# Kernel optimization log

Hardware: AMD Instinct MI355X
Metric: run time of the kernel (lower is better)

Reference implementation:

```python
import jax, jax.numpy as jnp
import numpy as np

D = 128           # embed_dim
NUM_LAYERS = 2
N_CLASSES = 4
OUT_CELL = 64
SPEAKERS = 2
INPUT_DIMS = [768, 74, 35]
B, T = 32, 60


def setup_inputs() -> dict:
    key = jax.random.key(0)
    ks = jax.random.split(key, 24)
    inp = {}
    inp['x0'] = jax.random.normal(ks[0], (B, T, INPUT_DIMS[0]), jnp.float32)
    inp['x1'] = jax.random.normal(ks[1], (B, T, INPUT_DIMS[1]), jnp.float32)
    inp['x2'] = jax.random.normal(ks[2], (B, T, INPUT_DIMS[2]), jnp.float32)
    inp['smask'] = jax.random.normal(ks[3], (B, T, SPEAKERS), jnp.float32)  # argmax -> speaker ids
    # modality projections
    for i, d in enumerate(INPUT_DIMS):
        inp[f'Wp{i}'] = jax.random.normal(ks[4 + i], (d, D), jnp.float32) / np.float32(np.sqrt(d))
        inp[f'bp{i}'] = jnp.zeros((D,), jnp.float32)
    # shared PositionEmbedding (ModuleList([m]*3) shares params)
    inp['freq_emb'] = jax.random.normal(ks[7], (SPEAKERS, D), jnp.float32) * 0.1
    inp['phase_emb'] = jax.random.normal(ks[8], (SPEAKERS, D), jnp.float32)
    # shared QRNNCell (ModuleList([cell]*num_layers) shares params)
    inp['U_x'] = jnp.linalg.qr(jax.random.normal(ks[9], (D, D), jnp.float32))[0]
    inp['U_h'] = jnp.linalg.qr(jax.random.normal(ks[10], (D, D), jnp.float32))[0]
    inp['Lambda'] = jnp.float32(0.5)
    # QMeasurement kernel (real/imag parts of D measurement vectors)
    inp['kernel_r'] = jnp.eye(D, dtype=jnp.float32) + 0.05 * jax.random.normal(ks[11], (D, D), jnp.float32)
    inp['kernel_i'] = 0.05 * jax.random.normal(ks[12], (D, D), jnp.float32)
    # SimpleNet fc_out
    inp['W1'] = jax.random.normal(ks[13], (D, OUT_CELL), jnp.float32) / np.float32(np.sqrt(D))
    inp['b1'] = jnp.zeros((OUT_CELL,), jnp.float32)
    inp['W2'] = jax.random.normal(ks[14], (OUT_CELL, N_CLASSES), jnp.float32) / np.float32(np.sqrt(OUT_CELL))
    inp['b2'] = jnp.zeros((N_CLASSES,), jnp.float32)
    return inp


def _qmn_forward(x0, x1, x2, smask, Wp0, bp0, Wp1, bp1, Wp2, bp2,
                 freq_emb, phase_emb, U_x, U_h, Lambda,
                 kernel_r, kernel_i, W1, b1, W2, b2):
    xs = [x0, x1, x2]
    Ws = [(Wp0, bp0), (Wp1, bp1), (Wp2, bp2)]
    reps = [jax.nn.relu(x @ W + b) for x, (W, b) in zip(xs, Ws)]           # [B,T,D] each
    # mixture weights: softmax over per-modality L2 norms
    norms = jnp.concatenate([jnp.linalg.norm(r, axis=-1, keepdims=True) for r in reps], axis=-1)
    weights = jax.nn.softmax(norms, axis=-1)                               # [B,T,M]
    # shared phase embedding: phase = t * freq[speaker] + phase[speaker]
    ids = jnp.argmax(smask, axis=-1)                                       # [B,T] int
    pos = jnp.arange(T, dtype=jnp.float32)[None, :, None]                  # [1,T,1]
    phase = pos * freq_emb[ids] + phase_emb[ids]                           # [B,T,D]
    cosp, sinp = jnp.cos(phase), jnp.sin(phase)
    # mixed density matrices rho = sum_m w_m |v_m><v_m|
    rho_r = jnp.zeros((B, T, D, D), jnp.float32)
    rho_i = jnp.zeros((B, T, D, D), jnp.float32)
    for m, r in enumerate(reps):
        a = r / jnp.maximum(jnp.linalg.norm(r, axis=-1, keepdims=True), 1e-12)
        pr = a * cosp                                                       # real amplitude
        pi = a * sinp                                                       # imag amplitude
        w = weights[..., m][..., None, None]
        rho_r = rho_r + w * (jnp.einsum('btm,btn->btmn', pr, pr) + jnp.einsum('btm,btn->btmn', pi, pi))
        rho_i = rho_i + w * (jnp.einsum('btm,btn->btmn', pi, pr) - jnp.einsum('btm,btn->btmn', pr, pi))
    # time-major for scan
    sr = jnp.transpose(rho_r, (1, 0, 2, 3))                                # [T,B,D,D]
    si = jnp.transpose(rho_i, (1, 0, 2, 3))

    def cell(h, x):
        hr, hi = h
        xr, xi = x
        Xr = jnp.einsum('mp,bpq,nq->bmn', U_x, xr, U_x)
        Xi = jnp.einsum('mp,bpq,nq->bmn', U_x, xi, U_x)
        Hr = jnp.einsum('mp,bpq,nq->bmn', U_h, hr, U_h)
        Hi = jnp.einsum('mp,bpq,nq->bmn', U_h, hi, U_h)
        nr = Lambda * Hr + (1.0 - Lambda) * Xr
        ni = Lambda * Hi + (1.0 - Lambda) * Xi
        return (nr, ni), (nr, ni)

    h0 = (jnp.broadcast_to(jnp.eye(D, dtype=jnp.float32) / D, (B, D, D)),
          jnp.zeros((B, D, D), jnp.float32))
    for _ in range(NUM_LAYERS):  # same shared cell params each layer
        _, (sr, si) = jax.lax.scan(cell, h0, (sr, si))
    # QMeasurement: p_k = Re(v_k^dag rho v_k), unit-norm complex measurement vectors
    nrm = jnp.sqrt(jnp.sum(kernel_r**2 + kernel_i**2, axis=1, keepdims=True))
    vr = kernel_r / jnp.maximum(nrm, 1e-12)                                # [K,D], K=D
    vi = kernel_i / jnp.maximum(nrm, 1e-12)
    probs = (jnp.einsum('tbmn,km,kn->tbk', sr, vr, vr)
             + jnp.einsum('tbmn,km,kn->tbk', sr, vi, vi)
             - jnp.einsum('tbmn,km,kn->tbk', si, vr, vi)
             + jnp.einsum('tbmn,km,kn->tbk', si, vi, vr))                  # [T,B,D]
    # SimpleNet (dropout = identity at inference)
    hid = jax.nn.relu(probs @ W1 + b1)
    out = jnp.tanh(hid @ W2 + b2)                                          # [T,B,C]
    out = jnp.transpose(out, (1, 0, 2))                                    # [B,T,C]
    return jax.nn.log_softmax(out, axis=2)


def reference(x0, x1, x2, smask, Wp0, bp0, Wp1, bp1, Wp2, bp2,
              freq_emb, phase_emb, U_x, U_h, Lambda,
              kernel_r, kernel_i, W1, b1, W2, b2):
    return _qmn_forward(x0, x1, x2, smask, Wp0, bp0, Wp1, bp1, Wp2, bp2,
                        freq_emb, phase_emb, U_x, U_h, Lambda,
                        kernel_r, kernel_i, W1, b1, W2, b2)
```

## Files before the change

### kernel.cpp

```cpp
#include <hip/hip_runtime.h>


#define DB 32
#define DT 60
#define DD 128
#define BT (DB*DT)
#define SP 136

typedef unsigned short ushort_t;
typedef __attribute__((ext_vector_type(8))) __bf16 bf16x8;
typedef __attribute__((ext_vector_type(8))) unsigned short ushort8_t;
typedef __attribute__((ext_vector_type(4))) float  float4v;

__device__ __forceinline__ float bf2f(ushort_t u){
  union { unsigned int i; float f; } x; x.i = ((unsigned int)u) << 16; return x.f;
}
__device__ __forceinline__ ushort_t f2bf(float f){
  union { float f; unsigned int i; } x; x.f = f;
  unsigned int lsb = (x.i >> 16) & 1u;
  return (ushort_t)((x.i + 0x7FFFu + lsb) >> 16);
}
__device__ __forceinline__ unsigned int f2bfpk(float a, float b){
#if defined(__gfx950__) && __has_builtin(__builtin_amdgcn_cvt_pk_bf16_f32)
  auto v = __builtin_amdgcn_cvt_pk_bf16_f32(a, b);
  unsigned int r; __builtin_memcpy(&r, &v, 4); return r;
#else
  return (unsigned int)f2bf(a) | ((unsigned int)f2bf(b) << 16);
#endif
}
__device__ __forceinline__ void split2(float v, ushort_t& h, ushort_t& l){
  h = f2bf(v); l = f2bf(v - bf2f(h));
}

template<int RT, int CT, bool ALO, bool BLO>
__device__ __forceinline__ void gemm_t(const ushort_t* Ah, const ushort_t* Al,
                                       const ushort_t* Bh, const ushort_t* Bl,
                                       float4v* acc, int row0, int col0, int gma, int q)
{
  for (int ks = 0; ks < 4; ks++){
    int ko = ks*32 + q*8;
    bf16x8 aF[RT], aL[RT], bF[CT], bL[CT];
    #pragma unroll
    for (int R = 0; R < RT; R++){
      int row = row0 + 16*R + gma;
      aF[R] = *(const bf16x8*)&Ah[row*SP + ko];
      if (ALO) aL[R] = *(const bf16x8*)&Al[row*SP + ko];
    }
    #pragma unroll
    for (int C = 0; C < CT; C++){
      int row = col0 + 16*C + gma;
      bF[C] = *(const bf16x8*)&Bh[row*SP + ko];
      if (BLO) bL[C] = *(const bf16x8*)&Bl[row*SP + ko];
    }
    #pragma unroll
    for (int R = 0; R < RT; R++)
      #pragma unroll
      for (int C = 0; C < CT; C++){
        float4v c = acc[R*CT+C];
        c = __builtin_amdgcn_mfma_f32_16x16x32_bf16(aF[R], bF[C], c, 0, 0, 0);
        if (BLO) c = __builtin_amdgcn_mfma_f32_16x16x32_bf16(aF[R], bL[C], c, 0, 0, 0);
        if (ALO) c = __builtin_amdgcn_mfma_f32_16x16x32_bf16(aL[R], bF[C], c, 0, 0, 0);
        acc[R*CT+C] = c;
      }
  }
}

template<int RT, int CT>
__device__ __forceinline__ void emit_t(const float4v* acc, ushort_t* dst, int stride,
                                       int row0, int col0, int gma, int q){
  #pragma unroll
  for (int R = 0; R < RT; R++)
    #pragma unroll
    for (int C = 0; C < CT; C++){
      int c = col0 + 16*C + gma, r0 = row0 + 16*R + 4*q;
      uint2 o;
      o.x = f2bfpk(acc[R*CT+C][0], acc[R*CT+C][1]);
      o.y = f2bfpk(acc[R*CT+C][2], acc[R*CT+C][3]);
      *(uint2*)&dst[(size_t)c*stride + r0] = o;
    }
}
template<int RT, int CT>
__device__ __forceinline__ void emit_split_t(const float4v* acc, ushort_t* dh, ushort_t* dl, int stride,
                                             int row0, int col0, int gma, int q){
  #pragma unroll
  for (int R = 0; R < RT; R++)
    #pragma unroll
    for (int C = 0; C < CT; C++){
      int c = col0 + 16*C + gma, r0 = row0 + 16*R + 4*q;
      ushort4 hh, ll;
      split2(acc[R*CT+C][0], hh.x, ll.x); split2(acc[R*CT+C][1], hh.y, ll.y);
      split2(acc[R*CT+C][2], hh.z, ll.z); split2(acc[R*CT+C][3], hh.w, ll.w);
      *(ushort4*)&dh[(size_t)c*stride + r0] = hh;
      *(ushort4*)&dl[(size_t)c*stride + r0] = ll;
    }
}
template<int NT>
__device__ __forceinline__ void lds_load_mat(ushort_t* dst, const ushort_t* src, int tid){
  for (int i = tid*8; i < 16384; i += NT*8){
    int r = i >> 7, k = i & 127;
    *(ushort8_t*)&dst[r*SP + k] = *(const ushort8_t*)&src[i];
  }
}
template<int NT>
__device__ __forceinline__ void lds_load_rows16(ushort_t* dst, const ushort_t* src, int tid){
  for (int i = tid*8; i < 2048; i += NT*8){
    int r = i >> 7, k = i & 127;
    *(ushort8_t*)&dst[r*SP + k] = *(const ushort8_t*)&src[i];
  }
}
template<int NT>
__device__ __forceinline__ void lds_load_mat2(ushort_t* d0, const ushort_t* s0,
                                              ushort_t* d1, const ushort_t* s1, int tid){
  constexpr int CH = 16384/(NT*8);
  ushort8_t r0[CH], r1[CH];
  #pragma unroll
  for (int c = 0; c < CH; c++) r0[c] = *(const ushort8_t*)&s0[tid*8 + c*NT*8];
  #pragma unroll
  for (int c = 0; c < CH; c++) r1[c] = *(const ushort8_t*)&s1[tid*8 + c*NT*8];
  #pragma unroll
  for (int c = 0; c < CH; c++){
    int i = tid*8 + c*NT*8; int r = i >> 7, k = i & 127;
    *(ushort8_t*)&d0[r*SP + k] = r0[c];
  }
  #pragma unroll
  for (int c = 0; c < CH; c++){
    int i = tid*8 + c*NT*8; int r = i >> 7, k = i & 127;
    *(ushort8_t*)&d1[r*SP + k] = r1[c];
  }
}
template<int NT>
__device__ __forceinline__ void lds_store_mat(ushort_t* dst, const ushort_t* src, int tid){
  for (int i = tid*8; i < 16384; i += NT*8){
    int r = i >> 7, k = i & 127;
    *(ushort8_t*)&dst[i] = *(const ushort8_t*)&src[r*SP + k];
  }
}

__device__ __forceinline__ void pow2_body(int blk2, int s,
    ushort_t* PpH, ushort_t* PpL, ushort_t* PTh, ushort_t* PTl,
    int tid, ushort_t* Ah, ushort_t* Al, ushort_t* Bh, ushort_t* Bl)
{
  int which = blk2 >> 3, sl = blk2 & 7;
  size_t src = (size_t)(s-1)*16384, dst = (size_t)s*16384;
  int gcol0 = sl*16;
  const ushort_t *A_h, *A_l, *B_h, *B_l; ushort_t *D_h, *D_l;
  if (which == 0){ A_h = PTh+src; A_l = PTl+src; B_h = PpH+src; B_l = PpL+src;
                   D_h = PpH+dst; D_l = PpL+dst; }
  else           { A_h = PpH+src; A_l = PpL+src; B_h = PTh+src; B_l = PTl+src;
                   D_h = PTh+dst; D_l = PTl+dst; }
  if (tid < 256){
    lds_load_mat<256>(Ah, A_h, tid);
    lds_load_mat<256>(Al, A_l, tid);
    lds_load_rows16<256>(Bh, B_h + (size_t)gcol0*128, tid);
    lds_load_rows16<256>(Bl, B_l + (size_t)gcol0*128, tid);
  }
  __syncthreads();
  if (tid < 256){
    int w = tid >> 6, lane = tid & 63, gma = lane & 15, q = lane >> 4;
    int row0 = 32*w;
    float4v acc[2];
    acc[0] = (float4v){0.f,0.f,0.f,0.f};
    acc[1] = (float4v){0.f,0.f,0.f,0.f};
    gemm_t<2,1,true,true>(Ah, Al, Bh, Bl, acc, row0, 0, gma, q);
    emit_split_t<2,1>(acc, D_h, D_l, 128, row0, gcol0, gma, q);
  }
}

__global__ void k_small(const float* Ux, const float* Uh, const float* kr, const float* ki,
                        const float* Wp0, const float* Wp1, const float* Wp2,
                        const float* x0, const float* x1, const float* x2,
                        ushort_t* UxTh, ushort_t* UxTl, ushort_t* UxH, ushort_t* UxL,
                        float* Vr, float* Vi,
                        ushort_t* PpH, ushort_t* PpL, ushort_t* PTh, ushort_t* PTl,
                        ushort_t* WT0h, ushort_t* WT0l, ushort_t* WT1h, ushort_t* WT1l,
                        ushort_t* WT2h, ushort_t* WT2l,
                        ushort_t* X0h, ushort_t* X0l, ushort_t* X1h, ushort_t* X1l,
                        ushort_t* X2h, ushort_t* X2l){
  int blk = blockIdx.x, d = threadIdx.x;
  if (blk < 128){
    int i = blk;
    float v = Ux[i*DD + d];
    ushort_t h, l; split2(v, h, l);
    UxTh[d*DD + i] = h; UxTl[d*DD + i] = l;
  } else if (blk < 256){
    __shared__ float red[DD];
    int k = blk - 128;
    float r = kr[k*DD+d], im = ki[k*DD+d];
    red[d] = r*r + im*im;
    __syncthreads();
    for (int s = 64; s > 0; s >>= 1){ if (d < s) red[d] += red[d+s]; __syncthreads(); }
    float nrm = fmaxf(sqrtf(red[0]), 1e-12f);
    Vr[k*DD+d] = r/nrm; Vi[k*DD+d] = im/nrm;
  } else if (blk < 384){
    int i = blk - 256;
    float v = Uh[i*DD + d];
    ushort_t h, l; split2(v, h, l);
    PpH[i*DD + d] = h;  PpL[i*DD + d] = l;
    PTh[d*DD + i] = h;  PTl[d*DD + i] = l;
  } else if (blk < 512){
    int dd2 = blk - 384;
    ushort_t h, l;
    for (int k = d; k < 768; k += 128){
      split2(Wp0[(size_t)k*DD + dd2], h, l);
      WT0h[(size_t)dd2*768 + k] = h; WT0l[(size_t)dd2*768 + k] = l;
    }
    { float v = (d < 74) ? Wp1[(size_t)d*DD + dd2] : 0.f;
      split2(v, h, l); WT1h[dd2*128 + d] = h; WT1l[dd2*128 + d] = l; }
    { float v = (d < 35) ? Wp2[(size_t)d*DD + dd2] : 0.f;
      split2(v, h, l); WT2h[dd2*128 + d] = h; WT2l[dd2*128 + d] = l; }
    { split2(Ux[(size_t)dd2*DD + d], h, l);
      UxH[dd2*DD + d] = h; UxL[dd2*DD + d] = l; }
  } else {
    int bt = blk - 512;
    ushort_t h, l;
    const float* r0 = x0 + (size_t)bt*768;
    #pragma unroll
    for (int j = 0; j < 6; j++){
      split2(r0[j*128 + d], h, l);
      X0h[(size_t)bt*768 + j*128 + d] = h;
      X0l[(size_t)bt*768 + j*128 + d] = l;
    }
    float v1 = (d < 74) ? x1[(size_t)bt*74 + d] : 0.f;
    split2(v1, h, l);
    X1h[(size_t)bt*128 + d] = h; X1l[(size_t)bt*128 + d] = l;
    float v2 = (d < 35) ? x2[(size_t)bt*35 + d] : 0.f;
    split2(v2, h, l);
    X2h[(size_t)bt*128 + d] = h; X2l[(size_t)bt*128 + d] = l;
  }
}

__global__ __launch_bounds__(512,1) void k_proj(
    const ushort_t* X0h, const ushort_t* X0l, const ushort_t* X1h, const ushort_t* X1l,
    const ushort_t* X2h, const ushort_t* X2l,
    const ushort_t* WT0h, const ushort_t* WT0l, const ushort_t* WT1h, const ushort_t* WT1l,
    const ushort_t* WT2h, const ushort_t* WT2l,
    const float* bp1, const float* bp2,
    float* Rpart, float* Reps,
    ushort_t* PpH, ushort_t* PpL, ushort_t* PTh, ushort_t* PTl)
{
  __shared__ ushort_t Ah[128*SP], Al[128*SP], Bh[128*SP], Bl[128*SP];
  int blk = blockIdx.x;
  int tid = threadIdx.x;
  if (blk >= 120){
    pow2_body(blk - 120, 1, PpH, PpL, PTh, PTl, tid, Ah, Al, Bh, Bl);
    return;
  }
  int m, tile, ch;
  if (blk < 90){ m = 0; tile = blk/6; ch = blk%6; }
  else if (blk < 105){ m = 1; tile = blk-90; ch = 0; }
  else { m = 2; tile = blk-105; ch = 0; }
  int bt0 = tile*128;
  int w = tid >> 6, lane = tid & 63, gma = lane & 15, q = lane >> 4;
  int row0 = 32*(w >> 1), col0 = 64*(w & 1);
  const ushort_t* Wh_ = (m==0)? WT0h : (m==1)? WT1h : WT2h;
  const ushort_t* Wl_ = (m==0)? WT0l : (m==1)? WT1l : WT2l;
  const ushort_t* Xh_ = (m==0)? X0h : (m==1)? X1h : X2h;
  const ushort_t* Xl_ = (m==0)? X0l : (m==1)? X1l : X2l;
  int KX = (m==0)? 768 : 128;
  for (int i = tid*8; i < 16384; i += 4096){
    int r = i >> 7, k = i & 127;
    *(ushort8_t*)&Ah[r*SP + k] = *(const ushort8_t*)&Wh_[(size_t)r*KX + ch*128 + k];
    *(ushort8_t*)&Al[r*SP + k] = *(const ushort8_t*)&Wl_[(size_t)r*KX + ch*128 + k];
    *(ushort8_t*)&Bh[r*SP + k] = *(const ushort8_t*)&Xh_[(size_t)(bt0+r)*KX + ch*128 + k];
    *(ushort8_t*)&Bl[r*SP + k] = *(const ushort8_t*)&Xl_[(size_t)(bt0+r)*KX + ch*128 + k];
  }
  __syncthreads();
  float4v acc[8];
  #pragma unroll
  for (int i = 0; i < 8; i++) acc[i] = (float4v){0.f,0.f,0.f,0.f};
  gemm_t<2,4,true,true>(Ah, Al, Bh, Bl, acc, row0, col0, gma, q);
  if (m == 0){
    #pragma unroll
    for (int R = 0; R < 2; R++)
      #pragma unroll
      for (int C = 0; C < 4; C++){
        int c = col0 + 16*C + gma, r0 = row0 + 16*R + 4*q;
        float4 o;
        o.x = acc[R*4+C][0]; o.y = acc[R*4+C][1];
        o.z = acc[R*4+C][2]; o.w = acc[R*4+C][3];
        *(float4*)&Rpart[((size_t)ch*BT + bt0 + c)*128 + r0] = o;
      }
  } else {
    const float* bp = (m==1)? bp1 : bp2;
    #pragma unroll
    for (int R = 0; R < 2; R++){
      int r0 = row0 + 16*R + 4*q;
      float4 bv = *(const float4*)&bp[r0];
      #pragma unroll
      for (int C = 0; C < 4; C++){
        int c = col0 + 16*C + gma;
        float4v a = acc[R*4+C];
        float4 o;
        o.x = fmaxf(a[0]+bv.x, 0.f); o.y = fmaxf(a[1]+bv.y, 0.f);
        o.z = fmaxf(a[2]+bv.z, 0.f); o.w = fmaxf(a[3]+bv.w, 0.f);
        *(float4*)&Reps[(size_t)(bt0 + c)*384 + m*128 + r0] = o;
      }
    }
  }
}

__global__ __launch_bounds__(128) void k_mix(const float* Rpart, const float* Reps,
    const float* bp0, const float* smask,
    const float* freq, const float* phem, ushort_t* PsH, ushort_t* PsL, float* Wgt)
{
  __shared__ float part[2][3];
  int bt = blockIdx.x; int t = bt % DT;
  int d = threadIdx.x;
  float r0v = bp0[d];
  #pragma unroll
  for (int ch = 0; ch < 6; ch++)
    r0v += Rpart[((size_t)ch*BT + bt)*128 + d];
  r0v = fmaxf(r0v, 0.f);
  float r1v = Reps[(size_t)bt*384 + 128 + d];
  float r2v = Reps[(size_t)bt*384 + 256 + d];
  float s0 = r0v*r0v, s1 = r1v*r1v, s2 = r2v*r2v;
  #pragma unroll
  for (int off = 1; off < 64; off <<= 1){
    s0 += __shfl_xor(s0, off, 64);
    s1 += __shfl_xor(s1, off, 64);
    s2 += __shfl_xor(s2, off, 64);
  }
  int wv = d >> 6;
  if ((d & 63) == 0){ part[wv][0] = s0; part[wv][1] = s1; part[wv][2] = s2; }
  __syncthreads();
  float n0 = sqrtf(part[0][0] + part[1][0]);
  float n1 = sqrtf(part[0][1] + part[1][1]);
  float n2 = sqrtf(part[0][2] + part[1][2]);
  float mx = fmaxf(n0, fmaxf(n1, n2));
  float e0 = expf(n0-mx), e1 = expf(n1-mx), e2 = expf(n2-mx);
  float einv = 1.f/(e0+e1+e2);
  if (d < 3) Wgt[bt*3+d] = (d==0?e0:(d==1?e1:e2))*einv;
  float sm0 = smask[bt*2], sm1 = smask[bt*2+1];
  int id = (sm1 > sm0) ? 1 : 0;
  float ph = (float)t * freq[id*DD+d] + phem[id*DD+d];
  float cp = cosf(ph), sp = sinf(ph);
  float a0 = r0v / fmaxf(n0, 1e-12f);
  float a1 = r1v / fmaxf(n1, 1e-12f);
  float a2 = r2v / fmaxf(n2, 1e-12f);
  ushort_t h, l;
  split2(a0*cp, h, l); PsH[((size_t)0*BT + bt)*DD + d] = h; PsL[((size_t)0*BT + bt)*DD + d] = l;
  split2(a1*cp, h, l); PsH[((size_t)1*BT + bt)*DD + d] = h; PsL[((size_t)1*BT + bt)*DD + d] = l;
  split2(a2*cp, h, l); PsH[((size_t)2*BT + bt)*DD + d] = h; PsL[((size_t)2*BT + bt)*DD + d] = l;
  split2(a0*sp, h, l); PsH[((size_t)3*BT + bt)*DD + d] = h; PsL[((size_t)3*BT + bt)*DD + d] = l;
  split2(a1*sp, h, l); PsH[((size_t)4*BT + bt)*DD + d] = h; PsL[((size_t)4*BT + bt)*DD + d] = l;
  split2(a2*sp, h, l); PsH[((size_t)5*BT + bt)*DD + d] = h; PsL[((size_t)5*BT + bt)*DD + d] = l;
}

__global__ __launch_bounds__(512,1) void k_qtrans(const ushort_t* UxH, const ushort_t* UxL,
                                                  const ushort_t* PsH, const ushort_t* PsL,
                                                  ushort_t* Qb,
                                                  ushort_t* PpH, ushort_t* PpL,
                                                  ushort_t* PTh, ushort_t* PTl){
  __shared__ ushort_t Ah[128*SP], Al[128*SP], Bh[128*SP], Bl[128*SP];
  int blk = blockIdx.x;
  int tid = threadIdx.x;
  if (blk >= 90){
    pow2_body(blk - 90, 2, PpH, PpL, PTh, PTl, tid, Ah, Al, Bh, Bl);
    return;
  }
  int w = tid >> 6, lane = tid & 63, gma = lane & 15, q = lane >> 4;
  int row0 = 32*(w >> 1), col0 = 64*(w & 1);
  size_t rbase = (size_t)blk*128*128;
  lds_load_mat<512>(Ah, UxH, tid);
  lds_load_mat<512>(Al, UxL, tid);
  lds_load_mat<512>(Bh, PsH + rbase, tid);
  lds_load_mat<512>(Bl, PsL + rbase, tid);
  __syncthreads();
  float4v acc[8];
  #pragma unroll
  for (int i = 0; i < 8; i++) acc[i] = (float4v){0.f,0.f,0.f,0.f};
  gemm_t<2,4,true,true>(Ah, Al, Bh, Bl, acc, row0, col0, gma, q);
  emit_t<2,4>(acc, Qb + rbase, 128, row0, col0, gma, q);
}

__global__ __launch_bounds__(256,2) void k_pow2v2(ushort_t* PpH, ushort_t* PpL,
                                                  ushort_t* PTh, ushort_t* PTl, int s){
  __shared__ ushort_t Ah[128*SP], Al[128*SP], Bh[16*SP], Bl[16*SP];
  int blk = blockIdx.x;
  int which = blk >> 3, sl = blk & 7;
  size_t src = (size_t)(s-1)*16384, dst = (size_t)s*16384;
  int tid = threadIdx.x;
  int w = tid >> 6, lane = tid & 63, gma = lane & 15, q = lane >> 4;
  int row0 = 32*w;
  int gcol0 = sl*16;
  const ushort_t *A_h, *A_l, *B_h, *B_l; ushort_t *D_h, *D_l;
  if (which == 0){ A_h = PTh+src; A_l = PTl+src; B_h = PpH+src; B_l = PpL+src;
                   D_h = PpH+dst; D_l = PpL+dst; }
  else           { A_h = PpH+src; A_l = PpL+src; B_h = PTh+src; B_l = PTl+src;
                   D_h = PTh+dst; D_l = PTl+dst; }
  lds_load_mat<256>(Ah, A_h, tid);
  lds_load_mat<256>(Al, A_l, tid);
  lds_load_rows16<256>(Bh, B_h + (size_t)gcol0*128, tid);
  lds_load_rows16<256>(Bl, B_l + (size_t)gcol0*128, tid);
  __syncthreads();
  float4v acc[2];
  acc[0] = (float4v){0.f,0.f,0.f,0.f};
  acc[1] = (float4v){0.f,0.f,0.f,0.f};
  gemm_t<2,1,true,true>(Ah, Al, Bh, Bl, acc, row0, 0, gma, q);
  emit_split_t<2,1>(acc, D_h, D_l, 128, row0, gcol0, gma, q);
}

__global__ __launch_bounds__(512,1) void k_gchain(const ushort_t* PpH, const ushort_t* PpL,
                                                  const ushort_t* PTh, const ushort_t* PTl,
                                                  ushort_t* GTh, ushort_t* GTl){
  __shared__ ushort_t Ah[128*SP], Al[128*SP], Bh[128*SP], Bl[128*SP];
  int t = blockIdx.x;
  int tid = threadIdx.x;
  int w = tid >> 6, lane = tid & 63, gma = lane & 15, q = lane >> 4;
  int row0 = 32*(w >> 1), col0 = 64*(w & 1);
  size_t gslot = (size_t)t * 16384;
  if (t == 0){
    for (int i = tid*4; i < 16384; i += 2048){
      int r = i >> 7, k = i & 127;
      ushort4 zz; zz.x = zz.y = zz.z = zz.w = 0;
      *(ushort4*)&GTl[gslot + i] = zz;
      ushort4 oh;
      oh.x = (r == (k+0)) ? (ushort_t)0x3F80 : (ushort_t)0;
      oh.y = (r == (k+1)) ? (ushort_t)0x3F80 : (ushort_t)0;
      oh.z = (r == (k+2)) ? (ushort_t)0x3F80 : (ushort_t)0;
      oh.w = (r == (k+3)) ? (ushort_t)0x3F80 : (ushort_t)0;
      *(ushort4*)&GTh[gslot + i] = oh;
    }
    return;
  }
  int b0 = __ffs(t) - 1;
  int rem = t & ~(1 << b0);
  if (rem == 0){
    size_t ps = (size_t)b0 * 16384;
    for (int i = tid*4; i < 16384; i += 2048){
      *(ushort4*)&GTh[gslot + i] = *(const ushort4*)&PTh[ps + i];
      *(ushort4*)&GTl[gslot + i] = *(const ushort4*)&PTl[ps + i];
    }
    return;
  }
  lds_load_mat<512>(Ah, PpH + (size_t)b0*16384, tid);
  lds_load_mat<512>(Al, PpL + (size_t)b0*16384, tid);
  while (rem){
    int k = __ffs(rem) - 1;
    rem &= ~(1 << k);
    lds_load_mat<512>(Bh, PTh + (size_t)k*16384, tid);
    lds_load_mat<512>(Bl, PTl + (size_t)k*16384, tid);
    __syncthreads();
    float4v acc[8];
    #pragma unroll
    for (int i = 0; i < 8; i++) acc[i] = (float4v){0.f,0.f,0.f,0.f};
    if (rem){
      gemm_t<2,4,true,true>(Bh, Bl, Ah, Al, acc, row0, col0, gma, q);
      __syncthreads();
      emit_split_t<2,4>(acc, Ah, Al, SP, row0, col0, gma, q);
      __syncthreads();
    } else {
      gemm_t<2,4,true,true>(Ah, Al, Bh, Bl, acc, row0, col0, gma, q);
      emit_split_t<2,4>(acc, GTh + gslot, GTl + gslot, 128, row0, col0, gma, q);
    }
  }
}

__global__ __launch_bounds__(512,1) void k_mwvt(
    const ushort_t* GTh, const ushort_t* GTl,
    const ushort_t* UxTh, const ushort_t* UxTl,
    const float* Vr, const float* Vi,
    const ushort_t* Qb,
    ushort_t* Mh, ushort_t* Wh, ushort_t* At)
{
  __shared__ ushort_t LBUF[4*128*SP];
  int blk = blockIdx.x;
  int tid = threadIdx.x;
  if (blk < 180){
    ushort_t* Bh = LBUF;
    ushort_t* Bl = LBUF + 128*SP;
    ushort_t* Ah = LBUF + 2*128*SP;
    ushort_t* Al = LBUF + 3*128*SP;
    int w = tid >> 6, lane = tid & 63, gma = lane & 15, q = lane >> 4;
    int row0 = 64*(w >> 1), col0 = 64*(w & 1);
    if (blk < 60){
      int t = blk;
      if (tid < 256){
        lds_load_mat<256>(Bh, GTh + (size_t)t*16384, tid);
        lds_load_mat<256>(Bl, GTl + (size_t)t*16384, tid);
        lds_load_mat<256>(Ah, UxTh, tid);
        lds_load_mat<256>(Al, UxTl, tid);
      }
      __syncthreads();
      float4v acc[16];
      if (tid < 256){
        #pragma unroll
        for (int i = 0; i < 16; i++) acc[i] = (float4v){0.f,0.f,0.f,0.f};
        gemm_t<4,4,true,true>(Ah, Al, Bh, Bl, acc, row0, col0, gma, q);
      }
      __syncthreads();
      if (tid < 256) emit_split_t<4,4>(acc, Ah, Al, SP, row0, col0, gma, q);
      __syncthreads();
      if (tid < 256){
        #pragma unroll
        for (int i = 0; i < 16; i++) acc[i] = (float4v){0.f,0.f,0.f,0.f};
        gemm_t<4,4,true,true>(Bh, Bl, Ah, Al, acc, row0, col0, gma, q);
        #pragma unroll
        for (int R = 0; R < 4; R++)
          #pragma unroll
          for (int C = 0; C < 4; C++){
            int c = col0 + 16*C + gma, r0 = row0 + 16*R + 4*q;
            uint2 o;
            o.x = f2bfpk(acc[R*4+C][0], acc[R*4+C][1]);
            o.y = f2bfpk(acc[R*4+C][2], acc[R*4+C][3]);
            *(uint2*)&Mh[(size_t)t*16384 + c*128 + r0] = o;
          }
      }
    } else {
      int bx = blk - 60;
      int t = bx >> 1, which = bx & 1;
      if (tid < 256){
        lds_load_mat<256>(Ah, GTh + (size_t)t*16384, tid);
        lds_load_mat<256>(Al, GTl + (size_t)t*16384, tid);
        const float* V = which ? Vi : Vr;
        for (int i = tid; i < 16384; i += 256){
          int r = i >> 7, k = i & 127;
          ushort_t h, l; split2(V[i], h, l);
          Bh[r*SP + k] = h; Bl[r*SP + k] = l;
        }
      }
      __syncthreads();
      if (tid < 256){
        float4v acc[16];
        #pragma unroll
        for (int i = 0; i < 16; i++) acc[i] = (float4v){0.f,0.f,0.f,0.f};
        gemm_t<4,4,true,true>(Ah, Al, Bh, Bl, acc, row0, col0, gma, q);
        #pragma unroll
        for (int R = 0; R < 4; R++)
          #pragma unroll
          for (int C = 0; C < 4; C++){
            int c = col0 + 16*C + gma, r0 = row0 + 16*R + 4*q;
            uint2 o;
            o.x = f2bfpk(acc[R*4+C][0], acc[R*4+C][1]);
            o.y = f2bfpk(acc[R*4+C][2], acc[R*4+C][3]);
            *(uint2*)&Wh[(size_t)bx*16384 + c*128 + r0] = o;
          }
      }
    }
  } else {
    ushort_t* Ah = LBUF;
    ushort_t* Bs = LBUF + 128*SP;
    int t = blk - 180;
    int w = tid >> 6, lane = tid & 63, gma = lane & 15, q = lane >> 4;
    int row0 = (w & 3)*32, col0 = (w >> 2)*96;
    lds_load_mat<512>(Ah, GTh + (size_t)t*16384, tid);
    for (int i = tid*8; i < 192*128; i += 4096){
      int m = i >> 7, k = i & 127;
      int j = m >> 5, b = m & 31;
      *(ushort8_t*)&Bs[m*SP + k] =
        *(const ushort8_t*)&Qb[((size_t)(j*BT) + b*DT + t)*DD + k];
    }
    __syncthreads();
    float4v acc[12];
    #pragma unroll
    for (int i = 0; i < 12; i++) acc[i] = (float4v){0.f,0.f,0.f,0.f};
    gemm_t<2,6,false,false>(Ah, Ah, Bs, Bs, acc, row0, col0, gma, q);
    emit_t<2,6>(acc, At + (size_t)t*24576, 128, row0, col0, gma, q);
  }
}

__global__ __launch_bounds__(256) void k_zbuild(ushort_t* S, const ushort_t* At,
                                                const float* Wgt, const float* lamp){
  __shared__ ushort_t As[2][6*DD];
  __shared__ float wl[2][3];
  int blk = blockIdx.x;
  int b = blk >> 5, sl2 = blk & 31;
  int tid = threadIdx.x;
  int r = sl2*4 + (tid >> 6);
  int c = (tid*2) & 127;
  float lam = lamp[0];
  float z0 = 0.f, z1 = 0.f;
  size_t off = (size_t)sl2*512 + tid*2;
  ushort4 pre;
  float wpre = 0.f;
  int jj0 = 0, n0 = 0;
  if (tid < 192){
    int i = tid*4;
    jj0 = i >> 7; n0 = i & 127;
    pre = *(const ushort4*)&At[(size_t)(jj0*32 + b)*128 + n0];
  }
  if (tid < 3) wpre = Wgt[(b*DT)*3 + tid];
  for (int t = 0; t < DT; t++){
    int cur = t & 1;
    if (tid < 192) *(ushort4*)&As[cur][tid*4] = pre;
    if (tid < 3) wl[cur][tid] = wpre;
    __syncthreads();
    if (t+1 < DT){
      if (tid < 192)
        pre = *(const ushort4*)&At[(size_t)(t+1)*24576 + (size_t)(jj0*32 + b)*128 + n0];
      if (tid < 3) wpre = Wgt[(b*DT + t+1)*3 + tid];
    }
    float ar[6];
    #pragma unroll
    for (int jj = 0; jj < 6; jj++) ar[jj] = bf2f(As[cur][jj*128 + r]);
    float w0 = wl[cur][0], w1 = wl[cur][1], w2 = wl[cur][2];
    float cb[6];
    cb[0] = w0*(ar[0]+ar[3]); cb[1] = w1*(ar[1]+ar[4]); cb[2] = w2*(ar[2]+ar[5]);
    cb[3] = w0*(ar[3]-ar[0]); cb[4] = w1*(ar[4]-ar[1]); cb[5] = w2*(ar[5]-ar[2]);
    float y0 = 0.f, y1 = 0.f;
    #pragma unroll
    for (int jj = 0; jj < 6; jj++){
      unsigned int a2 = *(const unsigned int*)&As[cur][jj*128 + c];
      float w_ = cb[jj];
      y0 += w_*bf2f((ushort_t)(a2 & 0xFFFF));
      y1 += w_*bf2f((ushort_t)(a2 >> 16));
    }
    z0 = lam*z0 + y0; z1 = lam*z1 + y1;
    *(unsigned int*)&S[((size_t)(t*32 + b))*16384 + off] = f2bfpk(z0, z1);
  }
}

__global__ __launch_bounds__(512,2) void k_conjmid(ushort_t* S, const ushort_t* Mh,
                                                   const float* lamp){
  __shared__ ushort_t Bh[128*SP], Zs[128*SP];
  int raw = blockIdx.x;
  int g = raw & 7, t = raw >> 3;
  int tid = threadIdx.x;
  int w = tid >> 6, lane = tid & 63, gma = lane & 15, q = lane >> 4;
  int row0 = 32*(w >> 1), col0 = 64*(w & 1);
  size_t slot0 = (size_t)(t*32 + g*4) * 16384;
  lds_load_mat2<512>(Zs, S + slot0, Bh, Mh + (size_t)t*16384, tid);
  __syncthreads();
  float lam = lamp[0];
  float oml = 1.f - lam;
  float ct = powf(lam, (float)(t+1)) / 128.f;
  for (int ib = 0; ib < 4; ib++){
    size_t slot = slot0 + (size_t)ib*16384;
    ushort8_t znext[4];
    if (ib < 3){
      #pragma unroll
      for (int c = 0; c < 4; c++)
        znext[c] = *(const ushort8_t*)&S[slot + 16384 + tid*8 + c*4096];
    }
    float4v acc[8];
    #pragma unroll
    for (int i = 0; i < 8; i++) acc[i] = (float4v){0.f,0.f,0.f,0.f};
    gemm_t<2,4,false,false>(Zs, Zs, Bh, Bh, acc, row0, col0, gma, q);
    __syncthreads();
    emit_t<2,4>(acc, Zs, SP, row0, col0, gma, q);
    __syncthreads();
    #pragma unroll
    for (int i = 0; i < 8; i++) acc[i] = (float4v){0.f,0.f,0.f,0.f};
    gemm_t<2,4,false,false>(Zs, Zs, Bh, Bh, acc, row0, col0, gma, q);
    __syncthreads();
    #pragma unroll
    for (int R = 0; R < 2; R++)
      #pragma unroll
      for (int C = 0; C < 4; C++){
        int c = col0 + 16*C + gma, r0 = row0 + 16*R + 4*q;
        float v0 = oml*acc[R*4+C][0] + ((c == r0+0) ? ct : 0.f);
        float v1 = oml*acc[R*4+C][1] + ((c == r0+1) ? ct : 0.f);
        float v2 = oml*acc[R*4+C][2] + ((c == r0+2) ? ct : 0.f);
        float v3 = oml*acc[R*4+C][3] + ((c == r0+3) ? ct : 0.f);
        uint2 o; o.x = f2bfpk(v0, v1); o.y = f2bfpk(v2, v3);
        *(uint2*)&Zs[(size_t)c*SP + r0] = o;
      }
    __syncthreads();
    lds_store_mat<512>(S + slot, Zs, tid);
    if (ib < 3){
      __syncthreads();
      #pragma unroll
      for (int c = 0; c < 4; c++){
        int i = tid*8 + c*4096;
        int r = i >> 7, k = i & 127;
        *(ushort8_t*)&Zs[r*SP + k] = znext[c];
      }
      __syncthreads();
    }
  }
}

__device__ __forceinline__ void prefix_ph2(uint2& buf, bool doload,
                                           const ushort_t* Snext, ushort_t* Scur,
                                           float* a, float lam){
  uint2 u = buf;
  if (doload) buf = *(const uint2*)Snext;
  a[0] = lam*a[0] + bf2f((ushort_t)(u.x & 0xFFFF));
  a[1] = lam*a[1] + bf2f((ushort_t)(u.x >> 16));
  a[2] = lam*a[2] + bf2f((ushort_t)(u.y & 0xFFFF));
  a[3] = lam*a[3] + bf2f((ushort_t)(u.y >> 16));
  uint2 o;
  o.x = f2bfpk(a[0], a[1]); o.y = f2bfpk(a[2], a[3]);
  *(uint2*)Scur = o;
}
__global__ __launch_bounds__(128) void k_prefix(ushort_t* S, const float* lamp){
  int blk = blockIdx.x;
  int chain = blk >> 5, slab = blk & 31;
  int tid = threadIdx.x;
  size_t off = (size_t)slab*512 + tid*4;
  float lam = lamp[0];
  float a[4];
  #pragma unroll
  for (int i = 0; i < 4; i++) a[i] = 0.f;
  size_t addr = (size_t)chain*16384 + off;
  const size_t step = (size_t)32*16384;
  uint2 b0 = *(const uint2*)&S[addr];
  uint2 b1 = *(const uint2*)&S[addr + step];
  uint2 b2 = *(const uint2*)&S[addr + 2*step];
  uint2 b3 = *(const uint2*)&S[addr + 3*step];
  uint2 b4 = *(const uint2*)&S[addr + 4*step];
  uint2 b5 = *(const uint2*)&S[addr + 5*step];
  for (int t = 0; t < DT; t += 6){
    prefix_ph2(b0, t+6  < DT, &S[addr + 6*step], &S[addr], a, lam); addr += step;
    prefix_ph2(b1, t+7  < DT, &S[addr + 6*step], &S[addr], a, lam); addr += step;
    prefix_ph2(b2, t+8  < DT, &S[addr + 6*step], &S[addr], a, lam); addr += step;
    prefix_ph2(b3, t+9  < DT, &S[addr + 6*step], &S[addr], a, lam); addr += step;
    prefix_ph2(b4, t+10 < DT, &S[addr + 6*step], &S[addr], a, lam); addr += step;
    prefix_ph2(b5, t+11 < DT, &S[addr + 6*step], &S[addr], a, lam); addr += step;
  }
}

__global__ __launch_bounds__(512,2) void k_meas(const ushort_t* S, const ushort_t* Wh,
                                                const float* lamp, float* Probs){
  __shared__ ushort_t Vs[128*SP], Cs[128*SP];
  __shared__ float Pd[64];
  int raw = blockIdx.x;
  int g = raw & 7;
  int h = (raw >> 3) & 1;
  int t = raw >> 4;
  int tid = threadIdx.x;
  int w = tid >> 6, lane = tid & 63, gma = lane & 15, q = lane >> 4;
  int row0 = 16*(w >> 1);
  int col0 = 64*(w & 1);
  size_t wbase = (size_t)(t*2) * 16384;
  size_t slot0 = (size_t)(t*32 + g*4) * 16384;
  ushort8_t creg[4], vreg[4];
  #pragma unroll
  for (int c = 0; c < 4; c++)
    creg[c] = *(const ushort8_t*)&S[slot0 + tid*8 + c*4096];
  #pragma unroll
  for (int c = 0; c < 4; c++){
    int i = tid*8 + c*4096;
    int r = i >> 7, k = i & 127;
    size_t gsrc = wbase + ((r < 64) ? 0 : 16384) + (size_t)(64*h + (r & 63))*128 + k;
    vreg[c] = *(const ushort8_t*)&Wh[gsrc];
  }
  if (tid < 64) Pd[tid] = 0.f;
  #pragma unroll
  for (int c = 0; c < 4; c++){
    int i = tid*8 + c*4096;
    int r = i >> 7, k = i & 127;
    *(ushort8_t*)&Cs[r*SP + k] = creg[c];
    *(ushort8_t*)&Vs[r*SP + k] = vreg[c];
  }
  __syncthreads();
  float lam = lamp[0];
  float ct = powf(lam, (float)(t+1)) / 128.f;
  for (int ib = 0; ib < 4; ib++){
    if (ib < 3){
      size_t snx = slot0 + (size_t)(ib+1)*16384;
      #pragma unroll
      for (int c = 0; c < 4; c++)
        creg[c] = *(const ushort8_t*)&S[snx + tid*8 + c*4096];
    }
    float4v acc[8];
    #pragma unroll
    for (int i = 0; i < 8; i++) acc[i] = (float4v){0.f,0.f,0.f,0.f};
    #pragma unroll
    for (int ks = 0; ks < 4; ks++){
      int ko = ks*32 + q*8;
      bf16x8 aF0 = *(const bf16x8*)&Vs[(row0 + gma)*SP + ko];
      bf16x8 aF1 = *(const bf16x8*)&Vs[(row0 + 64 + gma)*SP + ko];
      bf16x8 bF[4];
      #pragma unroll
      for (int C = 0; C < 4; C++)
        bF[C] = *(const bf16x8*)&Cs[(col0 + 16*C + gma)*SP + ko];
      #pragma unroll
      for (int C = 0; C < 4; C++){
        acc[C]   = __builtin_amdgcn_mfma_f32_16x16x32_bf16(aF0, bF[C], acc[C],   0, 0, 0);
        acc[4+C] = __builtin_amdgcn_mfma_f32_16x16x32_bf16(aF1, bF[C], acc[4+C], 0, 0, 0);
      }
    }
    #pragma unroll
    for (int j = 0; j < 4; j++){
      int kr = row0 + 4*q + j;
      float s = 0.f;
      #pragma unroll
      for (int C = 0; C < 4; C++){
        int m = col0 + 16*C + gma;
        float w0 = bf2f(Vs[kr*SP + m]);
        float w1 = bf2f(Vs[(kr + 64)*SP + m]);
        s += acc[C][j]*(w0 + w1) + acc[4+C][j]*(w1 - w0);
      }
      #pragma unroll
      for (int off = 1; off < 16; off <<= 1)
        s += __shfl_xor(s, off, 64);
      if (gma == 0) atomicAdd(&Pd[kr], s);
    }
    __syncthreads();
    if (tid < 64){
      Probs[(size_t)(t*32 + g*4 + ib)*DD + 64*h + tid] = (1.f - lam)*Pd[tid] + ct;
      Pd[tid] = 0.f;
    }
    if (ib < 3){
      #pragma unroll
      for (int c = 0; c < 4; c++){
        int i = tid*8 + c*4096;
        int r = i >> 7, k = i & 127;
        *(ushort8_t*)&Cs[r*SP + k] = creg[c];
      }
    }
    __syncthreads();
  }
}

__global__ __launch_bounds__(64) void k_head(const float* Probs, const float* W1, const float* b1,
                        const float* W2, const float* b2, float* out)
{
  __shared__ float ps[DD];
  __shared__ float hid[64];
  __shared__ float ov[4];
  int tb = blockIdx.x;
  int tid = threadIdx.x;
  ps[tid] = Probs[(size_t)tb*DD + tid];
  ps[tid+64] = Probs[(size_t)tb*DD + 64 + tid];
  __syncthreads();
  float acc = b1[tid];
  for (int dd = 0; dd < DD; dd++) acc += ps[dd]*W1[dd*64 + tid];
  hid[tid] = fmaxf(acc, 0.f);
  __syncthreads();
  if (tid < 4){
    float o = b2[tid];
    for (int j = 0; j < 64; j++) o += hid[j]*W2[j*4 + tid];
    ov[tid] = tanhf(o);
  }
  __syncthreads();
  if (tid == 0){
    float m = fmaxf(fmaxf(ov[0],ov[1]), fmaxf(ov[2],ov[3]));
    float lse = logf(expf(ov[0]-m)+expf(ov[1]-m)+expf(ov[2]-m)+expf(ov[3]-m));
    int t = tb >> 5, b = tb & 31;
    float* o = out + ((size_t)(b*DT + t))*4;
    o[0] = ov[0]-m-lse; o[1] = ov[1]-m-lse;
    o[2] = ov[2]-m-lse; o[3] = ov[3]-m-lse;
  }
}

extern "C" void kernel_launch(void* const* d_in, const int* in_sizes, int n_in,
                              void* d_out, int out_size, void* d_ws, size_t ws_size,
                              hipStream_t stream)
{
  const float* x0    = (const float*)d_in[0];
  const float* x1    = (const float*)d_in[1];
  const float* x2    = (const float*)d_in[2];
  const float* smask = (const float*)d_in[3];
  const float* Wp0   = (const float*)d_in[4];
  const float* bp0   = (const float*)d_in[5];
  const float* Wp1   = (const float*)d_in[6];
  const float* bp1   = (const float*)d_in[7];
  const float* Wp2   = (const float*)d_in[8];
  const float* bp2   = (const float*)d_in[9];
  const float* freq  = (const float*)d_in[10];
  const float* phem  = (const float*)d_in[11];
  const float* Ux    = (const float*)d_in[12];
  const float* Uh    = (const float*)d_in[13];
  const float* lamp  = (const float*)d_in[14];
  const float* kr    = (const float*)d_in[15];
  const float* ki    = (const float*)d_in[16];
  const float* W1    = (const float*)d_in[17];
  const float* b1    = (const float*)d_in[18];
  const float* W2    = (const float*)d_in[19];
  const float* b2    = (const float*)d_in[20];

  char* ws = (char*)d_ws;
  auto alignup = [](size_t x){ return (x + 255) & ~(size_t)255; };
  size_t off = 0;
  ushort_t* S   = (ushort_t*)(ws + off); off = alignup(off + (size_t)1920*16384*sizeof(ushort_t));
  ushort_t* Qb  = (ushort_t*)(ws + off); off = alignup(off + (size_t)6*BT*DD*sizeof(ushort_t));
  float* Rpart  = (float*)(ws + off);    off = alignup(off + (size_t)6*BT*DD*sizeof(float));
  float* Reps   = (float*)(ws + off);    off = alignup(off + (size_t)BT*384*sizeof(float));
  ushort_t* PsH = (ushort_t*)(ws + off); off = alignup(off + (size_t)6*BT*DD*sizeof(ushort_t));
  ushort_t* PsL = (ushort_t*)(ws + off); off = alignup(off + (size_t)6*BT*DD*sizeof(ushort_t));
  ushort_t* X0h = (ushort_t*)(ws + off); off = alignup(off + (size_t)BT*768*sizeof(ushort_t));
  ushort_t* X0l = (ushort_t*)(ws + off); off = alignup(off + (size_t)BT*768*sizeof(ushort_t));
  ushort_t* X1h = (ushort_t*)(ws + off); off = alignup(off + (size_t)BT*128*sizeof(ushort_t));
  ushort_t* X1l = (ushort_t*)(ws + off); off = alignup(off + (size_t)BT*128*sizeof(ushort_t));
  ushort_t* X2h = (ushort_t*)(ws + off); off = alignup(off + (size_t)BT*128*sizeof(ushort_t));
  ushort_t* X2l = (ushort_t*)(ws + off); off = alignup(off + (size_t)BT*128*sizeof(ushort_t));
  float* Wgt    = (float*)(ws + off);    off = alignup(off + (size_t)BT*3*sizeof(float));
  float* Vr     = (float*)(ws + off);    off = alignup(off + (size_t)DD*DD*sizeof(float));
  float* Vi     = (float*)(ws + off);    off = alignup(off + (size_t)DD*DD*sizeof(float));
  ushort_t* UxTh = (ushort_t*)(ws + off); off = alignup(off + (size_t)DD*DD*sizeof(ushort_t));
  ushort_t* UxTl = (ushort_t*)(ws + off); off = alignup(off + (size_t)DD*DD*sizeof(ushort_t));
  ushort_t* UxH = (ushort_t*)(ws + off); off = alignup(off + (size_t)DD*DD*sizeof(ushort_t));
  ushort_t* UxL = (ushort_t*)(ws + off); off = alignup(off + (size_t)DD*DD*sizeof(ushort_t));
  float* Probs  = (float*)(ws + off);    off = alignup(off + (size_t)BT*DD*sizeof(float));
  ushort_t* PpH = (ushort_t*)(ws + off); off = alignup(off + (size_t)6*16384*sizeof(ushort_t));
  ushort_t* PpL = (ushort_t*)(ws + off); off = alignup(off + (size_t)6*16384*sizeof(ushort_t));
  ushort_t* PTh = (ushort_t*)(ws + off); off = alignup(off + (size_t)6*16384*sizeof(ushort_t));
  ushort_t* PTl = (ushort_t*)(ws + off); off = alignup(off + (size_t)6*16384*sizeof(ushort_t));
  ushort_t* Mh  = (ushort_t*)(ws + off); off = alignup(off + (size_t)60*16384*sizeof(ushort_t));
  ushort_t* Wmh = (ushort_t*)(ws + off); off = alignup(off + (size_t)120*16384*sizeof(ushort_t));
  ushort_t* GTh = (ushort_t*)(ws + off); off = alignup(off + (size_t)60*16384*sizeof(ushort_t));
  ushort_t* GTl = (ushort_t*)(ws + off); off = alignup(off + (size_t)60*16384*sizeof(ushort_t));
  ushort_t* At  = (ushort_t*)(ws + off); off = alignup(off + (size_t)60*24576*sizeof(ushort_t));
  ushort_t* WT0h = (ushort_t*)(ws + off); off = alignup(off + (size_t)128*768*sizeof(ushort_t));
  ushort_t* WT0l = (ushort_t*)(ws + off); off = alignup(off + (size_t)128*768*sizeof(ushort_t));
  ushort_t* WT1h = (ushort_t*)(ws + off); off = alignup(off + (size_t)128*128*sizeof(ushort_t));
  ushort_t* WT1l = (ushort_t*)(ws + off); off = alignup(off + (size_t)128*128*sizeof(ushort_t));
  ushort_t* WT2h = (ushort_t*)(ws + off); off = alignup(off + (size_t)128*128*sizeof(ushort_t));
  ushort_t* WT2l = (ushort_t*)(ws + off); off = alignup(off + (size_t)128*128*sizeof(ushort_t));
  (void)ws_size; (void)in_sizes; (void)n_in; (void)out_size;

  k_small<<<512 + BT, 128, 0, stream>>>(Ux, Uh, kr, ki, Wp0, Wp1, Wp2, x0, x1, x2,
                                        UxTh, UxTl, UxH, UxL, Vr, Vi,
                                        PpH, PpL, PTh, PTl,
                                        WT0h, WT0l, WT1h, WT1l, WT2h, WT2l,
                                        X0h, X0l, X1h, X1l, X2h, X2l);
  k_proj<<<136, 512, 0, stream>>>(X0h, X0l, X1h, X1l, X2h, X2l,
                                  WT0h, WT0l, WT1h, WT1l, WT2h, WT2l,
                                  bp1, bp2, Rpart, Reps, PpH, PpL, PTh, PTl);
  k_mix<<<BT, 128, 0, stream>>>(Rpart, Reps, bp0, smask, freq, phem, PsH, PsL, Wgt);
  k_qtrans<<<106, 512, 0, stream>>>(UxH, UxL, PsH, PsL, Qb, PpH, PpL, PTh, PTl);
  for (int s = 3; s <= 5; s++)
    k_pow2v2<<<16, 256, 0, stream>>>(PpH, PpL, PTh, PTl, s);
  k_gchain<<<60, 512, 0, stream>>>(PpH, PpL, PTh, PTl, GTh, GTl);
  k_mwvt<<<240, 512, 0, stream>>>(GTh, GTl, UxTh, UxTl, Vr, Vi, Qb, Mh, Wmh, At);
  k_zbuild<<<1024, 256, 0, stream>>>(S, At, Wgt, lamp);
  k_conjmid<<<480, 512, 0, stream>>>(S, Mh, lamp);
  k_prefix<<<1024, 128, 0, stream>>>(S, lamp);
  k_meas<<<960, 512, 0, stream>>>(S, Wmh, lamp, Probs);
  k_head<<<BT, 64, 0, stream>>>(Probs, W1, b1, W2, b2, (float*)d_out);
}
```

Baseline: 296.2 us.

## Fuse power-doubling launches into cooperative gchain kernel and halve meas grid

Three small k_pow2v2 launches plus k_gchain become one cooperative kernel. It runs the power-doubling steps in its first 16 blocks and separates them with grid.sync, which removes launch gaps. k_meas now processes 8 batch slots per block instead of 4 across 480 blocks, so each block reuses its loaded measurement matrix more often. The costs are grid-sync overhead and lower parallelism in k_meas.

```diff
diff --git a/kernel.cpp b/kernel.cpp
--- a/kernel.cpp
+++ b/kernel.cpp
@@ -1,4 +1,5 @@
 #include <hip/hip_runtime.h>
+#include <hip/hip_cooperative_groups.h>
 
 
 #define DB 32
@@ -6,6 +7,8 @@
 #define DD 128
 #define BT (DB*DT)
 #define SP 136
+
+namespace cg = cooperative_groups;
 
 typedef unsigned short ushort_t;
 typedef __attribute__((ext_vector_type(8))) __bf16 bf16x8;
@@ -373,39 +376,18 @@
   emit_t<2,4>(acc, Qb + rbase, 128, row0, col0, gma, q);
 }
 
-__global__ __launch_bounds__(256,2) void k_pow2v2(ushort_t* PpH, ushort_t* PpL,
-                                                  ushort_t* PTh, ushort_t* PTl, int s){
-  __shared__ ushort_t Ah[128*SP], Al[128*SP], Bh[16*SP], Bl[16*SP];
-  int blk = blockIdx.x;
-  int which = blk >> 3, sl = blk & 7;
-  size_t src = (size_t)(s-1)*16384, dst = (size_t)s*16384;
-  int tid = threadIdx.x;
-  int w = tid >> 6, lane = tid & 63, gma = lane & 15, q = lane >> 4;
-  int row0 = 32*w;
-  int gcol0 = sl*16;
-  const ushort_t *A_h, *A_l, *B_h, *B_l; ushort_t *D_h, *D_l;
-  if (which == 0){ A_h = PTh+src; A_l = PTl+src; B_h = PpH+src; B_l = PpL+src;
-                   D_h = PpH+dst; D_l = PpL+dst; }
-  else           { A_h = PpH+src; A_l = PpL+src; B_h = PTh+src; B_l = PTl+src;
-                   D_h = PTh+dst; D_l = PTl+dst; }
-  lds_load_mat<256>(Ah, A_h, tid);
-  lds_load_mat<256>(Al, A_l, tid);
-  lds_load_rows16<256>(Bh, B_h + (size_t)gcol0*128, tid);
-  lds_load_rows16<256>(Bl, B_l + (size_t)gcol0*128, tid);
-  __syncthreads();
-  float4v acc[2];
-  acc[0] = (float4v){0.f,0.f,0.f,0.f};
-  acc[1] = (float4v){0.f,0.f,0.f,0.f};
-  gemm_t<2,1,true,true>(Ah, Al, Bh, Bl, acc, row0, 0, gma, q);
-  emit_split_t<2,1>(acc, D_h, D_l, 128, row0, gcol0, gma, q);
-}
-
-__global__ __launch_bounds__(512,1) void k_gchain(const ushort_t* PpH, const ushort_t* PpL,
-                                                  const ushort_t* PTh, const ushort_t* PTl,
-                                                  ushort_t* GTh, ushort_t* GTl){
+__global__ __launch_bounds__(512,1) void k_powgchain(
+    ushort_t* PpH, ushort_t* PpL, ushort_t* PTh, ushort_t* PTl,
+    ushort_t* GTh, ushort_t* GTl)
+{
   __shared__ ushort_t Ah[128*SP], Al[128*SP], Bh[128*SP], Bl[128*SP];
+  cg::grid_group grid = cg::this_grid();
   int t = blockIdx.x;
   int tid = threadIdx.x;
+  for (int s = 3; s <= 5; s++){
+    if (t < 16) pow2_body(t, s, PpH, PpL, PTh, PTl, tid, Ah, Al, Bh, Bl);
+    grid.sync();
+  }
   int w = tid >> 6, lane = tid & 63, gma = lane & 15, q = lane >> 4;
   int row0 = 32*(w >> 1), col0 = 64*(w & 1);
   size_t gslot = (size_t)t * 16384;
@@ -715,15 +697,15 @@
   __shared__ ushort_t Vs[128*SP], Cs[128*SP];
   __shared__ float Pd[64];
   int raw = blockIdx.x;
-  int g = raw & 7;
-  int h = (raw >> 3) & 1;
-  int t = raw >> 4;
+  int h = raw / 240;
+  int rem = raw % 240;
+  int t = rem >> 2, g = rem & 3;
   int tid = threadIdx.x;
   int w = tid >> 6, lane = tid & 63, gma = lane & 15, q = lane >> 4;
   int row0 = 16*(w >> 1);
   int col0 = 64*(w & 1);
   size_t wbase = (size_t)(t*2) * 16384;
-  size_t slot0 = (size_t)(t*32 + g*4) * 16384;
+  size_t slot0 = (size_t)(t*32 + g*8) * 16384;
   ushort8_t creg[4], vreg[4];
   #pragma unroll
   for (int c = 0; c < 4; c++)
@@ -746,8 +728,8 @@
   __syncthreads();
   float lam = lamp[0];
   float ct = powf(lam, (float)(t+1)) / 128.f;
-  for (int ib = 0; ib < 4; ib++){
-    if (ib < 3){
+  for (int ib = 0; ib < 8; ib++){
+    if (ib < 7){
       size_t snx = slot0 + (size_t)(ib+1)*16384;
       #pragma unroll
       for (int c = 0; c < 4; c++)
@@ -789,10 +771,10 @@
     }
     __syncthreads();
     if (tid < 64){
-      Probs[(size_t)(t*32 + g*4 + ib)*DD + 64*h + tid] = (1.f - lam)*Pd[tid] + ct;
+      Probs[(size_t)(t*32 + g*8 + ib)*DD + 64*h + tid] = (1.f - lam)*Pd[tid] + ct;
       Pd[tid] = 0.f;
     }
-    if (ib < 3){
+    if (ib < 7){
       #pragma unroll
       for (int c = 0; c < 4; c++){
         int i = tid*8 + c*4096;
@@ -911,13 +893,16 @@
                                   bp1, bp2, Rpart, Reps, PpH, PpL, PTh, PTl);
   k_mix<<<BT, 128, 0, stream>>>(Rpart, Reps, bp0, smask, freq, phem, PsH, PsL, Wgt);
   k_qtrans<<<106, 512, 0, stream>>>(UxH, UxL, PsH, PsL, Qb, PpH, PpL, PTh, PTl);
-  for (int s = 3; s <= 5; s++)
-    k_pow2v2<<<16, 256, 0, stream>>>(PpH, PpL, PTh, PTl, s);
-  k_gchain<<<60, 512, 0, stream>>>(PpH, PpL, PTh, PTl, GTh, GTl);
+  {
+    void* cargs[] = {(void*)&PpH, (void*)&PpL, (void*)&PTh, (void*)&PTl,
+                     (void*)&GTh, (void*)&GTl};
+    hipLaunchCooperativeKernel((const void*)k_powgchain, dim3(60), dim3(512),
+                               cargs, 0, stream);
+  }
   k_mwvt<<<240, 512, 0, stream>>>(GTh, GTl, UxTh, UxTl, Vr, Vi, Qb, Mh, Wmh, At);
   k_zbuild<<<1024, 256, 0, stream>>>(S, At, Wgt, lamp);
   k_conjmid<<<480, 512, 0, stream>>>(S, Mh, lamp);
   k_prefix<<<1024, 128, 0, stream>>>(S, lamp);
-  k_meas<<<960, 512, 0, stream>>>(S, Wmh, lamp, Probs);
+  k_meas<<<480, 512, 0, stream>>>(S, Wmh, lamp, Probs);
   k_head<<<BT, 64, 0, stream>>>(Probs, W1, b1, W2, b2, (float*)d_out);
 }
```

After: 352.1 us. 1.19x slower.
